# Kernel tuning notes

Hardware: AMD Instinct MI355X
Metric: run time of the kernel (lower is better)

The kernel has to match this reference:

```python
import jax, jax.numpy as jnp
import numpy as np

NUM_FIELDS = 50
CARD = 10000  # per-field cardinality; global index = x + field_offset
FACTOR_DIM = 64
ATT_SIZE = 64
BATCH = 2048


def setup_inputs() -> dict:
    key = jax.random.key(0)
    ks = jax.random.split(key, 5)
    x = jax.random.randint(ks[0], (BATCH, NUM_FIELDS), 0, CARD, dtype=jnp.int64)
    emb = jax.random.normal(ks[1], (NUM_FIELDS * CARD, FACTOR_DIM), jnp.float32) * 0.1
    W1 = jax.random.normal(ks[2], (FACTOR_DIM, ATT_SIZE), jnp.float32) * 0.1
    b1 = jnp.zeros((ATT_SIZE,), jnp.float32)
    w2 = jax.random.normal(ks[3], (ATT_SIZE, 1), jnp.float32) * 0.1
    b2 = jnp.zeros((1,), jnp.float32)
    lin_w = jax.random.normal(ks[4], (NUM_FIELDS * CARD, 1), jnp.float32) * 0.1
    lin_b = jnp.zeros((1,), jnp.float32)
    return {"x": x, "emb": emb, "W1": W1, "b1": b1, "w2": w2, "b2": b2,
            "lin_w": lin_w, "lin_b": lin_b}


def reference(x, emb, W1, b1, w2, b2, lin_w, lin_b):
    F = NUM_FIELDS
    offsets = (jnp.arange(F, dtype=x.dtype) * CARD)[None, :]  # [1, F]
    idx = x + offsets                                          # [B, F] global ids
    factors = emb[idx]                                         # [B, F, D]
    iu, ju = np.triu_indices(F, k=1)                           # P = F*(F-1)/2 pairs (i < j)
    inter = factors[:, iu, :] * factors[:, ju, :]              # [B, P, D]
    # attention MLP: Dense -> ReLU -> Dense(1) -> Softmax over pair axis
    h = jax.nn.relu(jnp.einsum('bpd,da->bpa', inter, W1) + b1)
    logits = jnp.einsum('bpa,ao->bpo', h, w2) + b2             # [B, P, 1]
    scores = jax.nn.softmax(logits, axis=1)
    inter_sum = jnp.sum(inter, axis=-1, keepdims=True)         # [B, P, 1]
    attended = jnp.sum(inter_sum * scores, axis=1)             # [B, 1]
    linear = jnp.sum(lin_w[idx], axis=1) + lin_b               # [B, 1]
    return linear + attended
```

## Files before the change

### kernel.cpp

```cpp
#include <hip/hip_runtime.h>
#include <hip/hip_bf16.h>

#define NF 50
#define NCARD 10000
#define FD 64
#define NPAIR 1225
#define NPAIR_PAD 1232
#define NTILE 77
#define NB 2
#define FROWB 144
#define FBATB 7200

typedef _Float16 h16x8 __attribute__((ext_vector_type(8)));
typedef float f32x4 __attribute__((ext_vector_type(4)));

__global__ void afm_pre(const float* __restrict__ W1,
                        _Float16* __restrict__ w1f,
                        unsigned* __restrict__ poffg) {
    const int bid = blockIdx.x, tid = threadIdx.x;
    if (bid < 2) {
        const int slot = bid * 4 + (tid >> 6);
        const int lane = tid & 63;
        const int n16 = lane & 15, quad = lane >> 4;
        const int mt = slot >> 1, ks = slot & 1;
        const int a = mt * 16 + n16;
        h16x8 v;
        #pragma unroll
        for (int jj = 0; jj < 8; ++jj) {
            int k = ks * 32 + quad * 8 + jj;
            v[jj] = (_Float16)W1[k * 64 + a];
        }
        *(h16x8*)(w1f + ((size_t)(slot * 64 + lane)) * 8) = v;
    } else {
        int p = (bid - 2) * 256 + tid;
        if (p < NPAIR_PAD) {
            int i = 0, j = 0;
            if (p < NPAIR) {
                float disc = (float)((2 * NF - 1) * (2 * NF - 1) - 8 * p);
                i = (int)(((float)(2 * NF - 1) - sqrtf(disc)) * 0.5f);
                if (i < 0) i = 0;
                if (i > NF - 2) i = NF - 2;
                while (i + 1 <= NF - 2 && (i + 1) * (NF - 1) - ((i + 1) * i) / 2 <= p) ++i;
                while (i > 0 && i * (NF - 1) - (i * (i - 1)) / 2 > p) --i;
                j = p - (i * (NF - 1) - (i * (i - 1)) / 2) + i + 1;
            }
            poffg[p] = (unsigned)(i * FROWB) | ((unsigned)(j * FROWB) << 16);
        }
    }
}

__global__ __launch_bounds__(256, 4) void afm_main(
    const int* __restrict__ x,
    const float* __restrict__ emb,
    const float* __restrict__ b1,
    const float* __restrict__ w2,
    const float* __restrict__ lin_w,
    const float* __restrict__ lin_b,
    const _Float16* __restrict__ w1f,
    const unsigned* __restrict__ poffg,
    float* __restrict__ out)
{
    __shared__ __align__(16) _Float16 fach[NB * 50 * 72];
    __shared__ unsigned poff[NPAIR_PAD];
    __shared__ float cmb[4][3];

    const int b0   = blockIdx.x * NB;
    const int tid  = threadIdx.x;
    const int lane = tid & 63;
    const int wid  = tid >> 6;
    const int n16  = lane & 15;
    const int quad = lane >> 4;

    for (int t = tid; t < NB * 50 * 8; t += 256) {
        int rowid = t >> 3, q = t & 7;
        int bb = (rowid >= 50) ? 1 : 0;
        int f = rowid - bb * 50;
        int gid = x[(b0 + bb) * NF + f] + f * NCARD;
        const float* src = emb + (size_t)gid * FD + q * 8;
        float4 v0 = *(const float4*)(src);
        float4 v1 = *(const float4*)(src + 4);
        h16x8 h;
        h[0] = (_Float16)v0.x; h[1] = (_Float16)v0.y;
        h[2] = (_Float16)v0.z; h[3] = (_Float16)v0.w;
        h[4] = (_Float16)v1.x; h[5] = (_Float16)v1.y;
        h[6] = (_Float16)v1.z; h[7] = (_Float16)v1.w;
        *(h16x8*)(fach + bb * 3600 + f * 72 + q * 8) = h;
    }
    for (int p = tid; p < NPAIR_PAD; p += 256) poff[p] = poffg[p];

    h16x8 afragW[8];
    #pragma unroll
    for (int s = 0; s < 8; ++s)
        afragW[s] = *(const h16x8*)(w1f + ((size_t)(s * 64 + lane)) * 8);
    h16x8 aones;
    {
        _Float16 o = (n16 == 0) ? (_Float16)1.0f : (_Float16)0.0f;
        #pragma unroll
        for (int jj = 0; jj < 8; ++jj) aones[jj] = o;
    }
    f32x4 b1v[4], w2v[4];
    #pragma unroll
    for (int mt = 0; mt < 4; ++mt) {
        const float4 bb = *(const float4*)(b1 + mt * 16 + quad * 4);
        const float4 ww = *(const float4*)(w2 + mt * 16 + quad * 4);
        b1v[mt] = (f32x4){bb.x, bb.y, bb.z, bb.w};
        w2v[mt] = (f32x4){ww.x, ww.y, ww.z, ww.w};
    }
    __syncthreads();

    const int mybatch = wid >> 1;
    const char* fb = (const char*)fach + mybatch * FBATB;
    float m = -1e30f, se = 0.f, sei = 0.f;

    for (int t = (wid & 1); t < NTILE; t += 2) {
        const unsigned po = poff[t * 16 + n16];
        const char* pbi = fb + (po & 0xFFFFu) + quad * 16;
        const char* pbj = fb + (po >> 16) + quad * 16;

        h16x8 fi0 = *(const h16x8*)(pbi);
        h16x8 fj0 = *(const h16x8*)(pbj);
        h16x8 fi1 = *(const h16x8*)(pbi + 64);
        h16x8 fj1 = *(const h16x8*)(pbj + 64);
        h16x8 pr0 = fi0 * fj0;
        h16x8 pr1 = fi1 * fj1;

        f32x4 acc[4];
        #pragma unroll
        for (int mt = 0; mt < 4; ++mt) {
            acc[mt] = __builtin_amdgcn_mfma_f32_16x16x32_f16(afragW[mt * 2 + 0], pr0, b1v[mt], 0, 0, 0);
            acc[mt] = __builtin_amdgcn_mfma_f32_16x16x32_f16(afragW[mt * 2 + 1], pr1, acc[mt], 0, 0, 0);
        }
        f32x4 accS = __builtin_amdgcn_mfma_f32_16x16x32_f16(aones, pr0, (f32x4){0.f, 0.f, 0.f, 0.f}, 0, 0, 0);
        accS = __builtin_amdgcn_mfma_f32_16x16x32_f16(aones, pr1, accS, 0, 0, 0);

        float lacc = 0.f;
        #pragma unroll
        for (int mt = 0; mt < 4; ++mt) {
            #pragma unroll
            for (int r = 0; r < 4; ++r)
                lacc += fmaxf(acc[mt][r], 0.f) * w2v[mt][r];
        }
        lacc += __shfl_xor(lacc, 16, 64);
        lacc += __shfl_xor(lacc, 32, 64);
        float is = __shfl(accS[0], n16, 64);

        if (t * 16 + n16 >= NPAIR) lacc = -1e30f;

        float nm = fmaxf(m, lacc);
        float sc = __expf(m - nm);
        float e  = __expf(lacc - nm);
        se  = se * sc + e;
        sei = sei * sc + e * is;
        m = nm;
    }

    #pragma unroll
    for (int d = 1; d <= 8; d <<= 1) {
        float m2   = __shfl_xor(m, d, 64);
        float se2  = __shfl_xor(se, d, 64);
        float sei2 = __shfl_xor(sei, d, 64);
        float nm = fmaxf(m, m2);
        float a = __expf(m - nm), bsc = __expf(m2 - nm);
        se  = se * a + se2 * bsc;
        sei = sei * a + sei2 * bsc;
        m = nm;
    }

    float lin = 0.f;
    if ((wid & 1) == 0) {
        if (lane < NF) {
            int gid = x[(b0 + mybatch) * NF + lane] + lane * NCARD;
            lin = lin_w[gid];
        }
        #pragma unroll
        for (int d = 1; d <= 32; d <<= 1) lin += __shfl_xor(lin, d, 64);
    }

    if (lane == 0) { cmb[wid][0] = m; cmb[wid][1] = se; cmb[wid][2] = sei; }
    __syncthreads();
    if ((wid & 1) == 0 && lane == 0) {
        float m2 = cmb[wid + 1][0], se2 = cmb[wid + 1][1], sei2 = cmb[wid + 1][2];
        float nm = fmaxf(m, m2);
        float a = __expf(m - nm), bsc = __expf(m2 - nm);
        float tse  = se * a + se2 * bsc;
        float tsei = sei * a + sei2 * bsc;
        out[b0 + mybatch] = lin + lin_b[0] + tsei / tse;
    }
}

extern "C" void kernel_launch(void* const* d_in, const int* in_sizes, int n_in,
                              void* d_out, int out_size, void* d_ws, size_t ws_size,
                              hipStream_t stream) {
    const int*   x     = (const int*)d_in[0];
    const float* emb   = (const float*)d_in[1];
    const float* W1    = (const float*)d_in[2];
    const float* b1    = (const float*)d_in[3];
    const float* w2    = (const float*)d_in[4];
    const float* lin_w = (const float*)d_in[6];
    const float* lin_b = (const float*)d_in[7];
    float* out = (float*)d_out;

    _Float16* w1f   = (_Float16*)d_ws;
    unsigned* poffg = (unsigned*)((char*)d_ws + 8192);

    afm_pre<<<7, 256, 0, stream>>>(W1, w1f, poffg);
    const int batch = out_size;
    afm_main<<<batch / NB, 256, 0, stream>>>(x, emb, b1, w2, lin_w, lin_b, w1f, poffg, out);
}
```

Before: 216.2 us.

## Fuse preprocessing into main kernel, pack ReLU-dot math, skip softmax rescale

Removes the separate preprocessing launch. Each block now computes the pair offset table and gathers and converts the W1 fragments itself, straight from global memory. The w2 dot product is rewritten as paired two-wide fma to encourage packed-math instructions. The online softmax skips the rescale exponential when no lane's logit exceeds the running max. The cost is redundant per-block work: the sqrt and loop index search plus 64 strided scalar W1 loads per thread. That work may cost more than the launch it removes.

```diff
diff --git a/kernel.cpp b/kernel.cpp
--- a/kernel.cpp
+++ b/kernel.cpp
@@ -1,5 +1,4 @@
 #include <hip/hip_runtime.h>
-#include <hip/hip_bf16.h>
 
 #define NF 50
 #define NCARD 10000
@@ -13,51 +12,16 @@
 
 typedef _Float16 h16x8 __attribute__((ext_vector_type(8)));
 typedef float f32x4 __attribute__((ext_vector_type(4)));
+typedef float f32x2 __attribute__((ext_vector_type(2)));
 
-__global__ void afm_pre(const float* __restrict__ W1,
-                        _Float16* __restrict__ w1f,
-                        unsigned* __restrict__ poffg) {
-    const int bid = blockIdx.x, tid = threadIdx.x;
-    if (bid < 2) {
-        const int slot = bid * 4 + (tid >> 6);
-        const int lane = tid & 63;
-        const int n16 = lane & 15, quad = lane >> 4;
-        const int mt = slot >> 1, ks = slot & 1;
-        const int a = mt * 16 + n16;
-        h16x8 v;
-        #pragma unroll
-        for (int jj = 0; jj < 8; ++jj) {
-            int k = ks * 32 + quad * 8 + jj;
-            v[jj] = (_Float16)W1[k * 64 + a];
-        }
-        *(h16x8*)(w1f + ((size_t)(slot * 64 + lane)) * 8) = v;
-    } else {
-        int p = (bid - 2) * 256 + tid;
-        if (p < NPAIR_PAD) {
-            int i = 0, j = 0;
-            if (p < NPAIR) {
-                float disc = (float)((2 * NF - 1) * (2 * NF - 1) - 8 * p);
-                i = (int)(((float)(2 * NF - 1) - sqrtf(disc)) * 0.5f);
-                if (i < 0) i = 0;
-                if (i > NF - 2) i = NF - 2;
-                while (i + 1 <= NF - 2 && (i + 1) * (NF - 1) - ((i + 1) * i) / 2 <= p) ++i;
-                while (i > 0 && i * (NF - 1) - (i * (i - 1)) / 2 > p) --i;
-                j = p - (i * (NF - 1) - (i * (i - 1)) / 2) + i + 1;
-            }
-            poffg[p] = (unsigned)(i * FROWB) | ((unsigned)(j * FROWB) << 16);
-        }
-    }
-}
-
-__global__ __launch_bounds__(256, 4) void afm_main(
+__global__ __launch_bounds__(256, 4) void afm_fused(
     const int* __restrict__ x,
     const float* __restrict__ emb,
+    const float* __restrict__ W1,
     const float* __restrict__ b1,
     const float* __restrict__ w2,
     const float* __restrict__ lin_w,
     const float* __restrict__ lin_b,
-    const _Float16* __restrict__ w1f,
-    const unsigned* __restrict__ poffg,
     float* __restrict__ out)
 {
     __shared__ __align__(16) _Float16 fach[NB * 50 * 72];
@@ -86,25 +50,47 @@
         h[6] = (_Float16)v1.z; h[7] = (_Float16)v1.w;
         *(h16x8*)(fach + bb * 3600 + f * 72 + q * 8) = h;
     }
-    for (int p = tid; p < NPAIR_PAD; p += 256) poff[p] = poffg[p];
+
+    for (int p = tid; p < NPAIR_PAD; p += 256) {
+        int i = 0, j = 0;
+        if (p < NPAIR) {
+            float disc = (float)((2 * NF - 1) * (2 * NF - 1) - 8 * p);
+            i = (int)(((float)(2 * NF - 1) - sqrtf(disc)) * 0.5f);
+            if (i < 0) i = 0;
+            if (i > NF - 2) i = NF - 2;
+            while (i + 1 <= NF - 2 && (i + 1) * (NF - 1) - ((i + 1) * i) / 2 <= p) ++i;
+            while (i > 0 && i * (NF - 1) - (i * (i - 1)) / 2 > p) --i;
+            j = p - (i * (NF - 1) - (i * (i - 1)) / 2) + i + 1;
+        }
+        poff[p] = (unsigned)(i * FROWB) | ((unsigned)(j * FROWB) << 16);
+    }
 
     h16x8 afragW[8];
     #pragma unroll
-    for (int s = 0; s < 8; ++s)
-        afragW[s] = *(const h16x8*)(w1f + ((size_t)(s * 64 + lane)) * 8);
+    for (int s = 0; s < 8; ++s) {
+        const int a  = (s >> 1) * 16 + n16;
+        const int kb = (s & 1) * 32 + quad * 8;
+        h16x8 v;
+        #pragma unroll
+        for (int jj = 0; jj < 8; ++jj)
+            v[jj] = (_Float16)W1[(kb + jj) * 64 + a];
+        afragW[s] = v;
+    }
     h16x8 aones;
     {
         _Float16 o = (n16 == 0) ? (_Float16)1.0f : (_Float16)0.0f;
         #pragma unroll
         for (int jj = 0; jj < 8; ++jj) aones[jj] = o;
     }
-    f32x4 b1v[4], w2v[4];
+    f32x4 b1v[4];
+    f32x2 w2lo[4], w2hi[4];
     #pragma unroll
     for (int mt = 0; mt < 4; ++mt) {
         const float4 bb = *(const float4*)(b1 + mt * 16 + quad * 4);
         const float4 ww = *(const float4*)(w2 + mt * 16 + quad * 4);
-        b1v[mt] = (f32x4){bb.x, bb.y, bb.z, bb.w};
-        w2v[mt] = (f32x4){ww.x, ww.y, ww.z, ww.w};
+        b1v[mt]  = (f32x4){bb.x, bb.y, bb.z, bb.w};
+        w2lo[mt] = (f32x2){ww.x, ww.y};
+        w2hi[mt] = (f32x2){ww.z, ww.w};
     }
     __syncthreads();
 
@@ -133,25 +119,33 @@
         f32x4 accS = __builtin_amdgcn_mfma_f32_16x16x32_f16(aones, pr0, (f32x4){0.f, 0.f, 0.f, 0.f}, 0, 0, 0);
         accS = __builtin_amdgcn_mfma_f32_16x16x32_f16(aones, pr1, accS, 0, 0, 0);
 
-        float lacc = 0.f;
+        f32x2 l2 = (f32x2){0.f, 0.f};
         #pragma unroll
         for (int mt = 0; mt < 4; ++mt) {
-            #pragma unroll
-            for (int r = 0; r < 4; ++r)
-                lacc += fmaxf(acc[mt][r], 0.f) * w2v[mt][r];
+            f32x2 r0 = (f32x2){fmaxf(acc[mt][0], 0.f), fmaxf(acc[mt][1], 0.f)};
+            f32x2 r1 = (f32x2){fmaxf(acc[mt][2], 0.f), fmaxf(acc[mt][3], 0.f)};
+            l2 = r0 * w2lo[mt] + l2;
+            l2 = r1 * w2hi[mt] + l2;
         }
+        float lacc = l2[0] + l2[1];
         lacc += __shfl_xor(lacc, 16, 64);
         lacc += __shfl_xor(lacc, 32, 64);
         float is = __shfl(accS[0], n16, 64);
 
         if (t * 16 + n16 >= NPAIR) lacc = -1e30f;
 
-        float nm = fmaxf(m, lacc);
-        float sc = __expf(m - nm);
-        float e  = __expf(lacc - nm);
-        se  = se * sc + e;
-        sei = sei * sc + e * is;
-        m = nm;
+        if (__all(lacc <= m)) {
+            float e = __expf(lacc - m);
+            se  += e;
+            sei += e * is;
+        } else {
+            float nm = fmaxf(m, lacc);
+            float sc = __expf(m - nm);
+            float e  = __expf(lacc - nm);
+            se  = se * sc + e;
+            sei = sei * sc + e * is;
+            m = nm;
+        }
     }
 
     #pragma unroll
@@ -200,10 +194,6 @@
     const float* lin_b = (const float*)d_in[7];
     float* out = (float*)d_out;
 
-    _Float16* w1f   = (_Float16*)d_ws;
-    unsigned* poffg = (unsigned*)((char*)d_ws + 8192);
-
-    afm_pre<<<7, 256, 0, stream>>>(W1, w1f, poffg);
     const int batch = out_size;
-    afm_main<<<batch / NB, 256, 0, stream>>>(x, emb, b1, w2, lin_w, lin_b, w1f, poffg, out);
+    afm_fused<<<batch / NB, 256, 0, stream>>>(x, emb, W1, b1, w2, lin_w, lin_b, out);
 }
```

After: 211.7 us. 1.02x faster.
